# Kernel tuning notes

Measured on AMD Instinct MI355X. Metric: run time of the kernel, lower is better.

## Reference

```python
import jax, jax.numpy as jnp
import numpy as np
from jax import lax

N_CLS = 4
ALPHA = 1.0
EPS = 1e-4


def _level_loss(logit, prob_gt, coord_gt, weight_cls):
    # logit: [B, N_cls*A, D, H, W]; prob_gt: [B, A, D, H, W]; coord_gt: [B, K, 4] int
    B, C, D, H, W = logit.shape
    A = C // N_CLS
    logit6 = logit.reshape(B, N_CLS, A, D, H, W)
    prob = jnp.clip(jax.nn.sigmoid(logit6), EPS, 1.0 - EPS)  # [B,N_cls,A,D,H,W]
    prob_max = jnp.max(prob, axis=1)                          # [B,A,D,H,W]

    # --- negative (background) focal term with NMS peak masking ---
    negmask = (prob_gt == -1.0).astype(logit.dtype)
    pooled = lax.reduce_window(prob_max, -jnp.inf, lax.max,
                               (1, 1, 3, 3, 3), (1, 1, 1, 1, 1),
                               [(0, 0), (0, 0), (1, 1), (1, 1), (1, 1)])
    max_filter = lax.stop_gradient((pooled == prob_max).astype(logit.dtype))
    thresh_filter = (prob_max > EPS).astype(logit.dtype)
    negmask = negmask * max_filter * thresh_filter
    w_neg = lax.stop_gradient(prob_max) ** ALPHA * negmask
    loss_neg = -jnp.sum(jnp.log(1.0 - prob_max) * w_neg)
    count_neg = jnp.sum(w_neg)

    # --- positive + other-class terms at sparse GT coordinates (vmapped over batch) ---
    def per_item(p_pred, l_pred, c_gt, p_gt):
        # p_pred/l_pred: [N_cls,A,D,H,W]; c_gt: [K,4]; p_gt: [A,D,H,W]
        valid = c_gt[:, 0] > -1
        vmask = valid.astype(p_pred.dtype)
        c = jnp.where(valid[:, None], c_gt, 0)  # safe indices for padded rows
        a, d, h, w = c[:, 0], c[:, 1], c[:, 2], c[:, 3]
        cls_gt = jnp.clip(p_gt[a, d, h, w].astype(jnp.int32) - 1, 0, N_CLS - 1)  # [K]
        p_t = p_pred[cls_gt, a, d, h, w]  # [K]
        l_t = l_pred[cls_gt, a, d, h, w]
        w_pos = (1.0 - lax.stop_gradient(p_t)) ** ALPHA * weight_cls[cls_gt] * vmask
        loss_pos = -jnp.sum(jax.nn.log_sigmoid(l_t) * w_pos)
        count_pos = jnp.sum(w_pos)
        # other-class suppression
        p_o = p_pred[:, a, d, h, w]  # [N_cls, K]
        l_o = l_pred[:, a, d, h, w]
        w_o = lax.stop_gradient(
            jax.nn.relu(p_o - (p_t - 0.05))
            * (p_o > 0.5).astype(p_o.dtype)
            * (p_t > 0.5).astype(p_o.dtype))
        # torch: weight[cls_gt] = 0  -> zero entire rows for classes present among valid GTs
        present = jnp.zeros((N_CLS,), p_pred.dtype).at[cls_gt].max(vmask)
        w_o = w_o * (1.0 - present)[:, None] * vmask[None, :]
        loss_other = jnp.sum(-jax.nn.log_sigmoid(-l_o) * w_o)
        count_other = jnp.sum(w_o)
        return loss_pos, count_pos, loss_other, count_other

    lp, cp, lo, co = jax.vmap(per_item)(prob, logit6, coord_gt, prob_gt)
    return (jnp.sum(lp), loss_neg, jnp.sum(lo), jnp.sum(cp), count_neg, jnp.sum(co))


def _forward(logits0, logits1, gtprob0, gtprob1, coords0, coords1, weight_cls):
    r0 = _level_loss(logits0, gtprob0, coords0, weight_cls)
    r1 = _level_loss(logits1, gtprob1, coords1, weight_cls)
    # [loss_pos, loss_neg, loss_other, count_pos, count_neg, count_other]
    return jnp.stack([a + b for a, b in zip(r0, r1)])


def setup_inputs() -> dict:
    rng = np.random.default_rng(0)
    B, A = 2, 2
    level_shapes = [(64, 128, 128), (32, 64, 64)]
    K, K_VALID = 32, 24
    out = {}
    for i, (D, H, W) in enumerate(level_shapes):
        logits = rng.standard_normal((B, N_CLS * A, D, H, W)).astype(np.float32)
        gt = -np.ones((B, A, D, H, W), np.float32)
        coords = -np.ones((B, K, 4), np.int32)
        for b in range(B):
            a = rng.integers(0, A, K_VALID)
            d = rng.integers(0, D, K_VALID)
            h = rng.integers(0, H, K_VALID)
            w = rng.integers(0, W, K_VALID)
            cls = rng.integers(1, N_CLS + 1, K_VALID)
            gt[b, a, d, h, w] = cls.astype(np.float32)
            coords[b, :K_VALID, 0] = a
            coords[b, :K_VALID, 1] = d
            coords[b, :K_VALID, 2] = h
            coords[b, :K_VALID, 3] = w
        out[f"logits{i}"] = jnp.asarray(logits)
        out[f"gtprob{i}"] = jnp.asarray(gt)
        out[f"coords{i}"] = jnp.asarray(coords)
    out["weight_cls"] = jnp.ones((N_CLS,), jnp.float32)
    return out


def reference(logits0, logits1, gtprob0, gtprob1, coords0, coords1, weight_cls):
    return _forward(logits0, logits1, gtprob0, gtprob1, coords0, coords1, weight_cls)
```

## Files before the change

### kernel.cpp

```cpp
#include <hip/hip_runtime.h>
#include <math.h>

#define EPSF 1e-4f

__device__ __forceinline__ float sigmoid_clip(float x) {
    float p = 1.0f / (1.0f + expf(-x));
    return fminf(fmaxf(p, EPSF), 1.0f - EPSF);
}

__device__ __forceinline__ float softplus(float x) {
    return fmaxf(x, 0.0f) + log1pf(expf(-fabsf(x)));
}


template <int W, int TY>
__global__ __launch_bounds__(W * TY) void neg_loss_kernel(
    const float* __restrict__ logits, const float* __restrict__ gtprob,
    double* __restrict__ ws, int A, int D, int H) {
    constexpr int LW = W + 2;
    __shared__ float pm[100 * LW];
    int tx = threadIdx.x, ty = threadIdx.y;
    int h0 = blockIdx.x * 8, d0 = blockIdx.y * 8;
    int ab = blockIdx.z;
    int a = ab % A, b = ab / A;
    size_t HW = (size_t)H * W;
    size_t vol = (size_t)D * HW;
    const float* lg = logits + ((size_t)b * 4 * A + a) * vol;
    size_t cs = (size_t)A * vol;

    for (int r = ty; r < 100; r += TY) {
        int dd = r / 10, hh = r - dd * 10;
        int d = d0 + dd - 1, h = h0 + hh - 1;
        float v = -INFINITY;
        if ((unsigned)d < (unsigned)D && (unsigned)h < (unsigned)H) {
            size_t off = (size_t)d * HW + (size_t)h * W + tx;
            float m0 = sigmoid_clip(lg[off]);
            float m1 = sigmoid_clip(lg[off + cs]);
            float m2 = sigmoid_clip(lg[off + 2 * cs]);
            float m3 = sigmoid_clip(lg[off + 3 * cs]);
            v = fmaxf(fmaxf(m0, m1), fmaxf(m2, m3));
        }
        pm[r * LW + tx + 1] = v;
        if (tx < 2) pm[r * LW + tx * (W + 1)] = -INFINITY;
    }
    __syncthreads();

    double lsum = 0.0, csum = 0.0;
    const float* gtb = gtprob + ((size_t)b * A + a) * vol;
    for (int hh = ty; hh < 8; hh += TY) {
        for (int dd = 0; dd < 8; dd++) {
            float pmc = pm[((dd + 1) * 10 + hh + 1) * LW + tx + 1];
            float mx = -INFINITY;
#pragma unroll
            for (int i = 0; i < 3; i++)
#pragma unroll
                for (int j = 0; j < 3; j++)
#pragma unroll
                    for (int l = 0; l < 3; l++)
                        mx = fmaxf(mx, pm[((dd + i) * 10 + hh + j) * LW + tx + l]);
            int d = d0 + dd, h = h0 + hh;
            float gt = gtb[(size_t)d * HW + (size_t)h * W + tx];
            if (gt == -1.0f && mx == pmc && pmc > EPSF) {
                lsum += (double)(-logf(1.0f - pmc) * pmc);
                csum += (double)pmc;
            }
        }
    }

    for (int o = 32; o > 0; o >>= 1) {
        lsum += __shfl_down(lsum, o);
        csum += __shfl_down(csum, o);
    }
    __shared__ double part[16];
    int tid = ty * W + tx;
    int wave = tid >> 6, lane = tid & 63;
    constexpr int NW = (W * TY) >> 6;
    if (lane == 0) { part[wave] = lsum; part[wave + NW] = csum; }
    __syncthreads();
    if (tid == 0) {
        double L = 0.0, C = 0.0;
#pragma unroll
        for (int i = 0; i < NW; i++) { L += part[i]; C += part[i + NW]; }
        atomicAdd(&ws[1], L);
        atomicAdd(&ws[4], C);
    }
}

__global__ __launch_bounds__(128) void pos_loss_kernel(
    const float* __restrict__ lg0, const float* __restrict__ gt0, const int* __restrict__ c0,
    const float* __restrict__ lg1, const float* __restrict__ gt1, const int* __restrict__ c1,
    const float* __restrict__ wcls, double* __restrict__ ws) {
    const int A = 2;
    int t = threadIdx.x;
    int lvl = t >> 6, tt = t & 63;
    int b = tt >> 5, k = tt & 31;
    const float* lg = lvl ? lg1 : lg0;
    const float* gt = lvl ? gt1 : gt0;
    const int* cd = lvl ? c1 : c0;
    int D = lvl ? 32 : 64, H = lvl ? 64 : 128, W = lvl ? 64 : 128;

    __shared__ unsigned present[4];
    if (t < 4) present[t] = 0u;
    __syncthreads();

    const int* c = cd + ((size_t)b * 32 + k) * 4;
    int a = c[0], d = c[1], h = c[2], w = c[3];
    bool valid = a > -1;
    if (!valid) { a = 0; d = 0; h = 0; w = 0; }
    size_t vol = (size_t)D * H * W;
    size_t off = ((size_t)d * H + h) * (size_t)W + w;
    float gval = gt[((size_t)b * A + a) * vol + off];
    int cls = (int)gval - 1;
    cls = cls < 0 ? 0 : (cls > 3 ? 3 : cls);
    if (valid) atomicOr(&present[lvl * 2 + b], 1u << cls);
    __syncthreads();
    unsigned pmask = present[lvl * 2 + b];

    float vm = valid ? 1.0f : 0.0f;
    const float* lgb = lg + (size_t)b * 4 * A * vol;
    size_t aoff = (size_t)a * vol + off;
    float l_t = lgb[(size_t)cls * A * vol + aoff];
    float p_t = sigmoid_clip(l_t);
    float w_pos = (1.0f - p_t) * wcls[cls] * vm;
    float loss_pos = softplus(-l_t) * w_pos;
    float pt_gate = (p_t > 0.5f) ? 1.0f : 0.0f;

    float loss_other = 0.0f, count_other = 0.0f;
#pragma unroll
    for (int cc = 0; cc < 4; cc++) {
        float l_o = lgb[(size_t)cc * A * vol + aoff];
        float p_o = sigmoid_clip(l_o);
        float wo = fmaxf(p_o - (p_t - 0.05f), 0.0f) * ((p_o > 0.5f) ? 1.0f : 0.0f) * pt_gate;
        float pres = ((pmask >> cc) & 1u) ? 1.0f : 0.0f;
        wo *= (1.0f - pres) * vm;
        loss_other += softplus(l_o) * wo;
        count_other += wo;
    }

    double v0 = (double)loss_pos, v1 = (double)w_pos, v2 = (double)loss_other, v3 = (double)count_other;
    for (int o = 32; o > 0; o >>= 1) {
        v0 += __shfl_down(v0, o);
        v1 += __shfl_down(v1, o);
        v2 += __shfl_down(v2, o);
        v3 += __shfl_down(v3, o);
    }
    __shared__ double part[8];
    int wave = t >> 6, lane = t & 63;
    if (lane == 0) {
        part[wave] = v0; part[wave + 2] = v1;
        part[wave + 4] = v2; part[wave + 6] = v3;
    }
    __syncthreads();
    if (t == 0) {
        atomicAdd(&ws[0], part[0] + part[1]);
        atomicAdd(&ws[3], part[2] + part[3]);
        atomicAdd(&ws[2], part[4] + part[5]);
        atomicAdd(&ws[5], part[6] + part[7]);
    }
}

__global__ void finalize_kernel(const double* __restrict__ ws, float* __restrict__ out) {
    int i = threadIdx.x;
    if (i < 6) out[i] = (float)ws[i];
}

extern "C" void kernel_launch(void* const* d_in, const int* in_sizes, int n_in,
                              void* d_out, int out_size, void* d_ws, size_t ws_size,
                              hipStream_t stream) {
    const float *logits0 = nullptr, *gtprob0 = nullptr, *logits1 = nullptr,
                *gtprob1 = nullptr, *wcls = nullptr;
    const int *coords0 = nullptr, *coords1 = nullptr;
    for (int i = 0; i < n_in; i++) {
        switch (in_sizes[i]) {
            case 16777216: logits0 = (const float*)d_in[i]; break;
            case 4194304:  gtprob0 = (const float*)d_in[i]; break;
            case 2097152:  logits1 = (const float*)d_in[i]; break;
            case 524288:   gtprob1 = (const float*)d_in[i]; break;
            case 4:        wcls    = (const float*)d_in[i]; break;
            case 256:
                if (!coords0) coords0 = (const int*)d_in[i];
                else          coords1 = (const int*)d_in[i];
                break;
        }
    }
    double* ws = (double*)d_ws;
    hipMemsetAsync(d_ws, 0, 6 * sizeof(double), stream);

    neg_loss_kernel<128, 4><<<dim3(16, 8, 4), dim3(128, 4), 0, stream>>>(
        logits0, gtprob0, ws, 2, 64, 128);
    neg_loss_kernel<64, 8><<<dim3(8, 4, 4), dim3(64, 8), 0, stream>>>(
        logits1, gtprob1, ws, 2, 32, 64);
    pos_loss_kernel<<<1, 128, 0, stream>>>(logits0, gtprob0, coords0,
                                           logits1, gtprob1, coords1, wcls, ws);
    finalize_kernel<<<1, 64, 0, stream>>>(ws, (float*)d_out);
}
```

Baseline: 173.3 us.

## Fuse all loss kernels into one launch with last-block reduction and finer tiles

Replaces the two negative-loss launches, the positive-loss launch and the finalize launch with a single kernel. Block 0 handles the sparse positive terms and the remaining blocks handle negative tiles with depth 4 instead of 8, which raises the block count. A last-block-done counter performs the final reduction in place of global double atomics. The kernel also applies one sigmoid to the max logit instead of four sigmoids, uses fast exp/rcp/log intrinsics, and reuses separable horizontal maxima across depth for the 3x3x3 pooling. The larger halo overhead per tile and the lower precision of the fast math could change the results slightly.

Measured after the change: 180.6 us. +4.2%, slower.

```diff
diff --git a/kernel.cpp b/kernel.cpp
--- a/kernel.cpp
+++ b/kernel.cpp
@@ -2,166 +2,210 @@
 #include <math.h>
 
 #define EPSF 1e-4f
-
-__device__ __forceinline__ float sigmoid_clip(float x) {
+#define NB_L1 256
+#define NB_L0 1024
+#define NBLK (1 + NB_L1 + NB_L0)
+
+static __device__ __forceinline__ float sigmoid_fast(float x) {
+    float e = __expf(-x);
+    float p = __builtin_amdgcn_rcpf(1.0f + e);
+    return fminf(fmaxf(p, EPSF), 1.0f - EPSF);
+}
+static __device__ __forceinline__ float sigmoid_precise(float x) {
     float p = 1.0f / (1.0f + expf(-x));
     return fminf(fmaxf(p, EPSF), 1.0f - EPSF);
 }
-
-__device__ __forceinline__ float softplus(float x) {
+static __device__ __forceinline__ float softplus(float x) {
     return fmaxf(x, 0.0f) + log1pf(expf(-fabsf(x)));
 }
 
-
-template <int W, int TY>
-__global__ __launch_bounds__(W * TY) void neg_loss_kernel(
-    const float* __restrict__ logits, const float* __restrict__ gtprob,
-    double* __restrict__ ws, int A, int D, int H) {
+template <int W>
+static __device__ __forceinline__ float hmax3(const float* pm, int rd, int hh, int tx) {
     constexpr int LW = W + 2;
-    __shared__ float pm[100 * LW];
-    int tx = threadIdx.x, ty = threadIdx.y;
-    int h0 = blockIdx.x * 8, d0 = blockIdx.y * 8;
-    int ab = blockIdx.z;
-    int a = ab % A, b = ab / A;
+    const float* p = pm + (rd * 10 + hh) * LW + tx;
+    float a = fmaxf(fmaxf(p[0], p[1]), p[2]);
+    float b = fmaxf(fmaxf(p[LW], p[LW + 1]), p[LW + 2]);
+    float c = fmaxf(fmaxf(p[2 * LW], p[2 * LW + 1]), p[2 * LW + 2]);
+    return fmaxf(fmaxf(a, b), c);
+}
+
+template <int W, int TY, int TD>
+static __device__ void neg_tile(const float* __restrict__ logits,
+                                const float* __restrict__ gtprob,
+                                int D, int H, int tileIdx, float* pm,
+                                double& lsum, double& csum) {
+    constexpr int LW = W + 2;
+    constexpr int NROW = (TD + 2) * 10;
+    const int A = 2;
+    const int nh = H / 8, nd = D / TD;
+    int ht = tileIdx % nh;
+    int rest = tileIdx / nh;
+    int dt = rest % nd;
+    int ab = rest / nd;
+    int a = ab & 1, b = ab >> 1;
+    int h0 = ht * 8, d0 = dt * TD;
     size_t HW = (size_t)H * W;
     size_t vol = (size_t)D * HW;
     const float* lg = logits + ((size_t)b * 4 * A + a) * vol;
     size_t cs = (size_t)A * vol;
-
-    for (int r = ty; r < 100; r += TY) {
+    const float* gtb = gtprob + ((size_t)b * A + a) * vol;
+    int tid = threadIdx.x;
+    int tx = tid % W, ty = tid / W;
+
+    for (int r = ty; r < NROW; r += TY) {
         int dd = r / 10, hh = r - dd * 10;
         int d = d0 + dd - 1, h = h0 + hh - 1;
         float v = -INFINITY;
         if ((unsigned)d < (unsigned)D && (unsigned)h < (unsigned)H) {
             size_t off = (size_t)d * HW + (size_t)h * W + tx;
-            float m0 = sigmoid_clip(lg[off]);
-            float m1 = sigmoid_clip(lg[off + cs]);
-            float m2 = sigmoid_clip(lg[off + 2 * cs]);
-            float m3 = sigmoid_clip(lg[off + 3 * cs]);
-            v = fmaxf(fmaxf(m0, m1), fmaxf(m2, m3));
+            float x = fmaxf(fmaxf(lg[off], lg[off + cs]),
+                            fmaxf(lg[off + 2 * cs], lg[off + 3 * cs]));
+            v = sigmoid_fast(x);
         }
         pm[r * LW + tx + 1] = v;
         if (tx < 2) pm[r * LW + tx * (W + 1)] = -INFINITY;
     }
     __syncthreads();
 
-    double lsum = 0.0, csum = 0.0;
-    const float* gtb = gtprob + ((size_t)b * A + a) * vol;
     for (int hh = ty; hh < 8; hh += TY) {
-        for (int dd = 0; dd < 8; dd++) {
+        float gtv[TD];
+#pragma unroll
+        for (int dd = 0; dd < TD; dd++)
+            gtv[dd] = gtb[(size_t)(d0 + dd) * HW + (size_t)(h0 + hh) * W + tx];
+        float hm0 = hmax3<W>(pm, 0, hh, tx);
+        float hm1 = hmax3<W>(pm, 1, hh, tx);
+#pragma unroll
+        for (int dd = 0; dd < TD; dd++) {
+            float hm2 = hmax3<W>(pm, dd + 2, hh, tx);
+            float mx = fmaxf(fmaxf(hm0, hm1), hm2);
             float pmc = pm[((dd + 1) * 10 + hh + 1) * LW + tx + 1];
-            float mx = -INFINITY;
-#pragma unroll
-            for (int i = 0; i < 3; i++)
-#pragma unroll
-                for (int j = 0; j < 3; j++)
-#pragma unroll
-                    for (int l = 0; l < 3; l++)
-                        mx = fmaxf(mx, pm[((dd + i) * 10 + hh + j) * LW + tx + l]);
-            int d = d0 + dd, h = h0 + hh;
-            float gt = gtb[(size_t)d * HW + (size_t)h * W + tx];
-            if (gt == -1.0f && mx == pmc && pmc > EPSF) {
-                lsum += (double)(-logf(1.0f - pmc) * pmc);
+            if (gtv[dd] == -1.0f && mx == pmc && pmc > EPSF) {
+                lsum += (double)(-__logf(1.0f - pmc) * pmc);
                 csum += (double)pmc;
             }
-        }
+            hm0 = hm1; hm1 = hm2;
+        }
+    }
+}
+
+__global__ __launch_bounds__(512) void fused_kernel(
+    const float* __restrict__ lg0, const float* __restrict__ gt0, const int* __restrict__ c0,
+    const float* __restrict__ lg1, const float* __restrict__ gt1, const int* __restrict__ c1,
+    const float* __restrict__ wcls, double* __restrict__ slots,
+    unsigned* __restrict__ counter, float* __restrict__ out) {
+    __shared__ float pm[60 * 130];
+    __shared__ double spart[48];
+    __shared__ unsigned present[4];
+    __shared__ bool isLast;
+    int tid = threadIdx.x;
+    int bid = blockIdx.x;
+    double v0 = 0, v1 = 0, v2 = 0, v3 = 0, v4 = 0, v5 = 0;
+
+    if (bid == 0) {
+        if (tid < 4) present[tid] = 0u;
+        __syncthreads();
+        int lvl = (tid >> 6) & 1, tt = tid & 63;
+        int b = tt >> 5, k = tt & 31;
+        const float* lg = lvl ? lg1 : lg0;
+        const float* gt = lvl ? gt1 : gt0;
+        const int* cd = lvl ? c1 : c0;
+        int D = lvl ? 32 : 64, H = lvl ? 64 : 128, Wd = lvl ? 64 : 128;
+        int a = 0, d = 0, h = 0, w = 0, cls = 0;
+        bool valid = false;
+        size_t vol = (size_t)D * H * Wd, off = 0;
+        if (tid < 128) {
+            const int* c = cd + ((size_t)b * 32 + k) * 4;
+            a = c[0]; d = c[1]; h = c[2]; w = c[3];
+            valid = a > -1;
+            if (!valid) { a = 0; d = 0; h = 0; w = 0; }
+            off = ((size_t)d * H + h) * (size_t)Wd + w;
+            float gval = gt[((size_t)b * 2 + a) * vol + off];
+            cls = (int)gval - 1;
+            cls = cls < 0 ? 0 : (cls > 3 ? 3 : cls);
+            if (valid) atomicOr(&present[lvl * 2 + b], 1u << cls);
+        }
+        __syncthreads();
+        if (tid < 128) {
+            unsigned pmask = present[lvl * 2 + b];
+            float vm = valid ? 1.0f : 0.0f;
+            const float* lgb = lg + (size_t)b * 8 * vol;
+            size_t aoff = (size_t)a * vol + off;
+            float l_t = lgb[(size_t)cls * 2 * vol + aoff];
+            float p_t = sigmoid_precise(l_t);
+            float w_pos = (1.0f - p_t) * wcls[cls] * vm;
+            float loss_pos = softplus(-l_t) * w_pos;
+            float ptg = (p_t > 0.5f) ? 1.0f : 0.0f;
+            float lo = 0.0f, co = 0.0f;
+#pragma unroll
+            for (int cc = 0; cc < 4; cc++) {
+                float l_o = lgb[(size_t)cc * 2 * vol + aoff];
+                float p_o = sigmoid_precise(l_o);
+                float wo = fmaxf(p_o - (p_t - 0.05f), 0.0f) * ((p_o > 0.5f) ? 1.0f : 0.0f) * ptg;
+                float pres = ((pmask >> cc) & 1u) ? 1.0f : 0.0f;
+                wo *= (1.0f - pres) * vm;
+                lo += softplus(l_o) * wo;
+                co += wo;
+            }
+            v0 = loss_pos; v3 = w_pos; v2 = lo; v5 = co;
+        }
+    } else if (bid <= NB_L1) {
+        neg_tile<64, 8, 4>(lg1, gt1, 32, 64, bid - 1, pm, v1, v4);
+    } else {
+        neg_tile<128, 4, 4>(lg0, gt0, 64, 128, bid - 1 - NB_L1, pm, v1, v4);
     }
 
     for (int o = 32; o > 0; o >>= 1) {
-        lsum += __shfl_down(lsum, o);
-        csum += __shfl_down(csum, o);
-    }
-    __shared__ double part[16];
-    int tid = ty * W + tx;
+        v0 += __shfl_down(v0, o); v1 += __shfl_down(v1, o); v2 += __shfl_down(v2, o);
+        v3 += __shfl_down(v3, o); v4 += __shfl_down(v4, o); v5 += __shfl_down(v5, o);
+    }
     int wave = tid >> 6, lane = tid & 63;
-    constexpr int NW = (W * TY) >> 6;
-    if (lane == 0) { part[wave] = lsum; part[wave + NW] = csum; }
+    if (lane == 0) {
+        double* sp = spart + wave * 6;
+        sp[0] = v0; sp[1] = v1; sp[2] = v2; sp[3] = v3; sp[4] = v4; sp[5] = v5;
+    }
     __syncthreads();
     if (tid == 0) {
-        double L = 0.0, C = 0.0;
-#pragma unroll
-        for (int i = 0; i < NW; i++) { L += part[i]; C += part[i + NW]; }
-        atomicAdd(&ws[1], L);
-        atomicAdd(&ws[4], C);
-    }
-}
-
-__global__ __launch_bounds__(128) void pos_loss_kernel(
-    const float* __restrict__ lg0, const float* __restrict__ gt0, const int* __restrict__ c0,
-    const float* __restrict__ lg1, const float* __restrict__ gt1, const int* __restrict__ c1,
-    const float* __restrict__ wcls, double* __restrict__ ws) {
-    const int A = 2;
-    int t = threadIdx.x;
-    int lvl = t >> 6, tt = t & 63;
-    int b = tt >> 5, k = tt & 31;
-    const float* lg = lvl ? lg1 : lg0;
-    const float* gt = lvl ? gt1 : gt0;
-    const int* cd = lvl ? c1 : c0;
-    int D = lvl ? 32 : 64, H = lvl ? 64 : 128, W = lvl ? 64 : 128;
-
-    __shared__ unsigned present[4];
-    if (t < 4) present[t] = 0u;
+        double s[6] = {0, 0, 0, 0, 0, 0};
+#pragma unroll
+        for (int wv = 0; wv < 8; wv++)
+#pragma unroll
+            for (int j = 0; j < 6; j++) s[j] += spart[wv * 6 + j];
+        double* slot = slots + (size_t)bid * 6;
+#pragma unroll
+        for (int j = 0; j < 6; j++) slot[j] = s[j];
+        __threadfence();
+        unsigned prev = atomicAdd(counter, 1u);
+        isLast = (prev == NBLK - 1);
+    }
     __syncthreads();
-
-    const int* c = cd + ((size_t)b * 32 + k) * 4;
-    int a = c[0], d = c[1], h = c[2], w = c[3];
-    bool valid = a > -1;
-    if (!valid) { a = 0; d = 0; h = 0; w = 0; }
-    size_t vol = (size_t)D * H * W;
-    size_t off = ((size_t)d * H + h) * (size_t)W + w;
-    float gval = gt[((size_t)b * A + a) * vol + off];
-    int cls = (int)gval - 1;
-    cls = cls < 0 ? 0 : (cls > 3 ? 3 : cls);
-    if (valid) atomicOr(&present[lvl * 2 + b], 1u << cls);
-    __syncthreads();
-    unsigned pmask = present[lvl * 2 + b];
-
-    float vm = valid ? 1.0f : 0.0f;
-    const float* lgb = lg + (size_t)b * 4 * A * vol;
-    size_t aoff = (size_t)a * vol + off;
-    float l_t = lgb[(size_t)cls * A * vol + aoff];
-    float p_t = sigmoid_clip(l_t);
-    float w_pos = (1.0f - p_t) * wcls[cls] * vm;
-    float loss_pos = softplus(-l_t) * w_pos;
-    float pt_gate = (p_t > 0.5f) ? 1.0f : 0.0f;
-
-    float loss_other = 0.0f, count_other = 0.0f;
-#pragma unroll
-    for (int cc = 0; cc < 4; cc++) {
-        float l_o = lgb[(size_t)cc * A * vol + aoff];
-        float p_o = sigmoid_clip(l_o);
-        float wo = fmaxf(p_o - (p_t - 0.05f), 0.0f) * ((p_o > 0.5f) ? 1.0f : 0.0f) * pt_gate;
-        float pres = ((pmask >> cc) & 1u) ? 1.0f : 0.0f;
-        wo *= (1.0f - pres) * vm;
-        loss_other += softplus(l_o) * wo;
-        count_other += wo;
-    }
-
-    double v0 = (double)loss_pos, v1 = (double)w_pos, v2 = (double)loss_other, v3 = (double)count_other;
-    for (int o = 32; o > 0; o >>= 1) {
-        v0 += __shfl_down(v0, o);
-        v1 += __shfl_down(v1, o);
-        v2 += __shfl_down(v2, o);
-        v3 += __shfl_down(v3, o);
-    }
-    __shared__ double part[8];
-    int wave = t >> 6, lane = t & 63;
-    if (lane == 0) {
-        part[wave] = v0; part[wave + 2] = v1;
-        part[wave + 4] = v2; part[wave + 6] = v3;
-    }
-    __syncthreads();
-    if (t == 0) {
-        atomicAdd(&ws[0], part[0] + part[1]);
-        atomicAdd(&ws[3], part[2] + part[3]);
-        atomicAdd(&ws[2], part[4] + part[5]);
-        atomicAdd(&ws[5], part[6] + part[7]);
-    }
-}
-
-__global__ void finalize_kernel(const double* __restrict__ ws, float* __restrict__ out) {
-    int i = threadIdx.x;
-    if (i < 6) out[i] = (float)ws[i];
+    if (isLast) {
+        __threadfence();
+        double acc[6] = {0, 0, 0, 0, 0, 0};
+        for (int i = tid; i < NBLK; i += 512) {
+            const double* sl = slots + (size_t)i * 6;
+#pragma unroll
+            for (int j = 0; j < 6; j++) acc[j] += sl[j];
+        }
+#pragma unroll
+        for (int j = 0; j < 6; j++)
+            for (int o = 32; o > 0; o >>= 1) acc[j] += __shfl_down(acc[j], o);
+        __syncthreads();
+        if (lane == 0) {
+            double* sp = spart + wave * 6;
+#pragma unroll
+            for (int j = 0; j < 6; j++) sp[j] = acc[j];
+        }
+        __syncthreads();
+        if (tid == 0) {
+#pragma unroll
+            for (int j = 0; j < 6; j++) {
+                double s = 0;
+#pragma unroll
+                for (int wv = 0; wv < 8; wv++) s += spart[wv * 6 + j];
+                out[j] = (float)s;
+            }
+        }
+    }
 }
 
 extern "C" void kernel_launch(void* const* d_in, const int* in_sizes, int n_in,
@@ -183,14 +227,10 @@
                 break;
         }
     }
-    double* ws = (double*)d_ws;
-    hipMemsetAsync(d_ws, 0, 6 * sizeof(double), stream);
-
-    neg_loss_kernel<128, 4><<<dim3(16, 8, 4), dim3(128, 4), 0, stream>>>(
-        logits0, gtprob0, ws, 2, 64, 128);
-    neg_loss_kernel<64, 8><<<dim3(8, 4, 4), dim3(64, 8), 0, stream>>>(
-        logits1, gtprob1, ws, 2, 32, 64);
-    pos_loss_kernel<<<1, 128, 0, stream>>>(logits0, gtprob0, coords0,
-                                           logits1, gtprob1, coords1, wcls, ws);
-    finalize_kernel<<<1, 64, 0, stream>>>(ws, (float*)d_out);
-}
+    unsigned* counter = (unsigned*)d_ws;
+    double* slots = (double*)((char*)d_ws + 64);
+    hipMemsetAsync(d_ws, 0, 64, stream);
+    fused_kernel<<<NBLK, 512, 0, stream>>>(logits0, gtprob0, coords0,
+                                           logits1, gtprob1, coords1,
+                                           wcls, slots, counter, (float*)d_out);
+}
```
